# Kernel optimization log

Hardware: AMD Instinct MI355X
Metric: run time of the kernel (lower is better)

Reference implementation:

```python
import jax, jax.numpy as jnp
import numpy as np

# Config constants (match init_kwargs)
D_MODEL = 1024
D_MLP = 2048
NUM_EXPERTS = 8
EXPERTS_PER_TOKEN = 2
BATCH, SEQ = 2, 2048


def setup_inputs() -> dict:
    key = jax.random.key(0)
    k0, k1, k2, k3, k4 = jax.random.split(key, 5)
    init = lambda k, shape: jax.random.normal(k, shape, jnp.float32) * 0.02
    return {
        "x": jax.random.normal(k0, (BATCH, SEQ, D_MODEL), jnp.float32),
        "W_router": init(k1, (D_MODEL, NUM_EXPERTS)),
        "W_gate": init(k2, (NUM_EXPERTS, D_MODEL, D_MLP)),
        "W_in": init(k3, (NUM_EXPERTS, D_MODEL, D_MLP)),
        "W_out": init(k4, (NUM_EXPERTS, D_MLP, D_MODEL)),
    }


def reference(x, W_router, W_gate, W_in, W_out):
    B, S, D = x.shape
    h = x.reshape(-1, D)                                  # [T, D]
    T = h.shape[0]
    E = W_router.shape[1]

    # Router: softmax in fp32, top-k, renormalize (as in torch source)
    router_logits = h @ W_router                          # [T, E]
    probs = jax.nn.softmax(router_logits.astype(jnp.float32), axis=-1)
    top_w, top_i = jax.lax.top_k(probs, EXPERTS_PER_TOKEN)  # [T, K]
    top_w = top_w / top_w.sum(axis=-1, keepdims=True)
    top_w = top_w.astype(h.dtype)

    # Dense combine matrix [T, E]; top-k indices are distinct per token
    combine = jnp.zeros((T, E), h.dtype).at[jnp.arange(T)[:, None], top_i].set(top_w)

    # GatedMLP per expert: silu(h @ Wg) * (h @ Wi) @ Wo  (computed densely over experts,
    # then combined with the sparse routing weights -> same math as gather/MLP/scatter loop)
    gate_pre = jnp.einsum('td,edf->etf', h, W_gate)       # [E, T, F]
    up = jnp.einsum('td,edf->etf', h, W_in)               # [E, T, F]
    act = jax.nn.silu(gate_pre) * up                      # [E, T, F]
    expert_out = jnp.einsum('etf,efd->etd', act, W_out)   # [E, T, D]

    out = jnp.einsum('etd,te->td', expert_out, combine)   # [T, D]
    return out.reshape(B, S, D), router_logits
```

## Files before the change

### kernel.cpp

```cpp
#include <hip/hip_runtime.h>
#include <cstdint>
#include <cstddef>

#define T_TOK 4096
#define DM 1024
#define DF 2048
#define NE 8
#define PADROWS 9216
#define MAXTILES 72

typedef unsigned short u16;
typedef unsigned int u32;
using short8 = __attribute__((ext_vector_type(8))) short;
using f32x4  = __attribute__((ext_vector_type(4))) float;

static constexpr size_t OFF_H    = 0;
static constexpr size_t OFF_WGT  = OFF_H   + (size_t)T_TOK * DM * 2;
static constexpr size_t OFF_WIT  = OFF_WGT + (size_t)NE * DM * DF * 2;
static constexpr size_t OFF_WOT  = OFF_WIT + (size_t)NE * DM * DF * 2;
static constexpr size_t OFF_A    = OFF_WOT + (size_t)NE * DF * DM * 2;
static constexpr size_t OFF_TOK  = OFF_A   + (size_t)PADROWS * DF * 2;
static constexpr size_t OFF_WL   = OFF_TOK + PADROWS * 4;
static constexpr size_t OFF_TEXP = OFF_WL  + PADROWS * 4;
static constexpr size_t OFF_TW   = OFF_TEXP + (size_t)T_TOK * 2 * 4;
static constexpr size_t OFF_CNT  = OFF_TW  + (size_t)T_TOK * 2 * 4;
static constexpr size_t OFF_CUR  = OFF_CNT + 64;
static constexpr size_t OFF_NT   = OFF_CUR + 64;
static constexpr size_t OFF_TE   = OFF_NT  + 64;
static constexpr size_t OFF_TP   = OFF_TE  + 512;
static constexpr size_t OFF_ZPG  = OFF_TP  + 512;
static constexpr size_t OFF_POS  = OFF_ZPG + 4096;

__device__ __forceinline__ u16 f2bf(float f) {
  u32 u = __builtin_bit_cast(u32, f);
  u += 0x7FFFu + ((u >> 16) & 1u);
  return (u16)(u >> 16);
}

__device__ __forceinline__ void async16(const void* g, void* l) {
  __builtin_amdgcn_global_load_lds((__attribute__((address_space(1))) void*)(g),
                                   (__attribute__((address_space(3))) void*)(l),
                                   16, 0, 0);
}

__global__ void convert_x_k(const float4* __restrict__ x, u16* __restrict__ h) {
  size_t i = (size_t)blockIdx.x * 256 + threadIdx.x;
  float4 v = x[i];
  u32 lo = (u32)f2bf(v.x) | ((u32)f2bf(v.y) << 16);
  u32 hi = (u32)f2bf(v.z) | ((u32)f2bf(v.w) << 16);
  uint2 o; o.x = lo; o.y = hi;
  *(uint2*)&h[i * 4] = o;
}

__global__ void init_small_k(int* __restrict__ tok, float* __restrict__ wl,
                             int* __restrict__ cnt, u16* __restrict__ zpg) {
  int i = blockIdx.x * 256 + threadIdx.x;
  if (i < PADROWS) { tok[i] = -1; wl[i] = 0.f; }
  if (i < NE) cnt[i] = 0;
  if (i < 2048) zpg[i] = 0;
}

__global__ void transpose_w_k(const float* __restrict__ Wg, const float* __restrict__ Wi,
                              const float* __restrict__ Wo, u16* __restrict__ wgT,
                              u16* __restrict__ wiT, u16* __restrict__ woT) {
  __shared__ u16 lT[64][65];
  int bid = blockIdx.x;
  int mat = bid >> 12;
  int r = bid & 4095;
  const float* src; u16* dst; int R, C;
  if (mat == 0)      { src = Wg; dst = wgT; R = DM; C = DF; }
  else if (mat == 1) { src = Wi; dst = wiT; R = DM; C = DF; }
  else               { src = Wo; dst = woT; R = DF; C = DM; }
  int e = r >> 9;
  int rem = r & 511;
  int ctiles = C >> 6;
  int tr = rem / ctiles, tc = rem % ctiles;
  size_t eb = (size_t)e * R * C;
  int r0 = tr * 64, c0 = tc * 64;
  int wv = threadIdx.x >> 6, lane = threadIdx.x & 63;
#pragma unroll
  for (int it = 0; it < 16; ++it) {
    int rl = it * 4 + wv;
    float v = src[eb + (size_t)(r0 + rl) * C + c0 + lane];
    lT[lane][rl] = f2bf(v);
  }
  __syncthreads();
#pragma unroll
  for (int it = 0; it < 16; ++it) {
    int cl = it * 4 + wv;
    dst[eb + (size_t)(c0 + cl) * R + r0 + lane] = lT[cl][lane];
  }
}

__global__ void router_k(const float* __restrict__ x, const float* __restrict__ Wr,
                         float* __restrict__ logits, int* __restrict__ texp,
                         float* __restrict__ tw, int* __restrict__ cnt) {
  int wv = threadIdx.x >> 6, lane = threadIdx.x & 63;
  int t = blockIdx.x * 4 + wv;
  const float* h = x + (size_t)t * DM;
  float acc[8] = {0.f, 0.f, 0.f, 0.f, 0.f, 0.f, 0.f, 0.f};
#pragma unroll
  for (int j = 0; j < 16; ++j) {
    float hv = h[lane + j * 64];
    const float4* wr = (const float4*)(Wr + (size_t)(lane + j * 64) * 8);
    float4 w0 = wr[0], w1 = wr[1];
    acc[0] += hv * w0.x; acc[1] += hv * w0.y; acc[2] += hv * w0.z; acc[3] += hv * w0.w;
    acc[4] += hv * w1.x; acc[5] += hv * w1.y; acc[6] += hv * w1.z; acc[7] += hv * w1.w;
  }
#pragma unroll
  for (int e = 0; e < 8; ++e)
#pragma unroll
    for (int off = 32; off > 0; off >>= 1) acc[e] += __shfl_down(acc[e], off, 64);
  if (lane == 0) {
    float mx = acc[0];
#pragma unroll
    for (int e = 1; e < 8; ++e) mx = fmaxf(mx, acc[e]);
    float p[8];
#pragma unroll
    for (int e = 0; e < 8; ++e) p[e] = __expf(acc[e] - mx);
    int i1 = 0; float b1 = p[0];
#pragma unroll
    for (int e = 1; e < 8; ++e) if (p[e] > b1) { b1 = p[e]; i1 = e; }
    int i2 = -1; float b2 = -1.f;
#pragma unroll
    for (int e = 0; e < 8; ++e) if (e != i1 && p[e] > b2) { b2 = p[e]; i2 = e; }
    float inv = 1.f / (b1 + b2);
    texp[t * 2] = i1; texp[t * 2 + 1] = i2;
    tw[t * 2] = b1 * inv; tw[t * 2 + 1] = b2 * inv;
    atomicAdd(&cnt[i1], 1); atomicAdd(&cnt[i2], 1);
#pragma unroll
    for (int e = 0; e < 8; ++e) logits[(size_t)t * 8 + e] = acc[e];
  }
}

__global__ void plan_k(const int* __restrict__ cnt, int* __restrict__ cursor,
                       int* __restrict__ tile_e, int* __restrict__ tile_p,
                       int* __restrict__ ntiles) {
  if (threadIdx.x == 0) {
    int off = 0, nt = 0;
    for (int e = 0; e < NE; ++e) {
      cursor[e] = off;
      int n = cnt[e];
      int t = (n + 127) >> 7;
      for (int i = 0; i < t; ++i) { tile_e[nt] = e; tile_p[nt] = off + i * 128; ++nt; }
      off += t * 128;
    }
    *ntiles = nt;
  }
}

__global__ void scatter_k(const int* __restrict__ texp, const float* __restrict__ tw,
                          int* __restrict__ cursor, int* __restrict__ tok,
                          float* __restrict__ wl, int* __restrict__ pos) {
  int t = blockIdx.x * 256 + threadIdx.x;
#pragma unroll
  for (int k = 0; k < 2; ++k) {
    int e = texp[t * 2 + k];
    int p = atomicAdd(&cursor[e], 1);
    tok[p] = t;
    wl[p] = tw[t * 2 + k];
    pos[t * 2 + k] = p;
  }
}

__global__ __launch_bounds__(256) void gemm1_k(
    const u16* __restrict__ hbf, const u16* __restrict__ wgT, const u16* __restrict__ wiT,
    const int* __restrict__ tok, const float* __restrict__ wl,
    const int* __restrict__ tile_e, const int* __restrict__ tile_p,
    const int* __restrict__ ntiles, const u16* __restrict__ zpg,
    u16* __restrict__ Aact) {
  __shared__ char smem[65536];
  const int tile = blockIdx.y;
  if (tile >= *ntiles) return;
  const int e  = tile_e[tile];
  const int p0 = tile_p[tile];
  const int f0 = blockIdx.x * 64;
  const int tid = threadIdx.x, wv = tid >> 6, lane = tid & 63;

  const u16* hsrc[4];
  int hoff[4];
#pragma unroll
  for (int i = 0; i < 4; ++i) {
    const int row = wv * 32 + i * 8 + (lane >> 3);
    const int gc  = (lane & 7) ^ (row & 7);
    const int tk  = tok[p0 + row];
    hsrc[i] = (tk >= 0) ? (hbf + (size_t)tk * DM + gc * 8) : (zpg + gc * 8);
    hoff[i] = (wv * 32 + i * 8) * 64;
  }
  const u16* wbase = ((wv < 2) ? wgT : wiT) + (size_t)e * DM * DF;
  const int half = wv & 1, mt = wv >> 1;
  const u16* bsrc[4];
  int boff[4];
#pragma unroll
  for (int i = 0; i < 4; ++i) {
    const int row = half * 32 + i * 8 + (lane >> 3);
    const int gc  = (lane & 7) ^ (row & 7);
    bsrc[i] = wbase + (size_t)(f0 + row) * DM + gc * 8;
    boff[i] = 8192 + mt * 4096 + (half * 32 + i * 8) * 64;
  }

  f32x4 accG[4][2], accU[4][2];
#pragma unroll
  for (int m = 0; m < 4; ++m)
#pragma unroll
    for (int n = 0; n < 2; ++n) { accG[m][n] = (f32x4)(0.f); accU[m][n] = (f32x4)(0.f); }

  const int wr = wv >> 1, wc = wv & 1;
  const int wrBase = wr * 64, wcBase = wc * 32;
  const int l4 = lane >> 4, ln = lane & 15;

  {
    u16* b = (u16*)smem;
#pragma unroll
    for (int i = 0; i < 4; ++i) async16(hsrc[i], b + hoff[i]);
#pragma unroll
    for (int i = 0; i < 4; ++i) async16(bsrc[i], b + boff[i]);
  }
  __syncthreads();

  int cur = 0;
  for (int kt = 0; kt < DM / 64; ++kt) {
    if (kt < DM / 64 - 1) {
      u16* b = (u16*)smem + (cur ^ 1) * 16384;
#pragma unroll
      for (int i = 0; i < 4; ++i) async16(hsrc[i] + (size_t)(kt + 1) * 64, b + hoff[i]);
#pragma unroll
      for (int i = 0; i < 4; ++i) async16(bsrc[i] + (size_t)(kt + 1) * 64, b + boff[i]);
    }
    const u16* b = (const u16*)smem + cur * 16384;
#pragma unroll
    for (int s = 0; s < 2; ++s) {
      const int c = s * 4 + l4;
      short8 a[4], bg[2], bu[2];
#pragma unroll
      for (int m = 0; m < 4; ++m) {
        const int row = wrBase + m * 16 + ln;
        a[m] = *(const short8*)&b[row * 64 + ((c ^ (row & 7)) * 8)];
      }
#pragma unroll
      for (int n = 0; n < 2; ++n) {
        const int rowb = wcBase + n * 16 + ln;
        const int so = rowb * 64 + ((c ^ (rowb & 7)) * 8);
        bg[n] = *(const short8*)&b[8192 + so];
        bu[n] = *(const short8*)&b[12288 + so];
      }
#pragma unroll
      for (int m = 0; m < 4; ++m)
#pragma unroll
        for (int n = 0; n < 2; ++n) {
          accG[m][n] = __builtin_amdgcn_mfma_f32_16x16x32_bf16(a[m], bg[n], accG[m][n], 0, 0, 0);
          accU[m][n] = __builtin_amdgcn_mfma_f32_16x16x32_bf16(a[m], bu[n], accU[m][n], 0, 0, 0);
        }
    }
    __syncthreads();
    cur ^= 1;
  }

  u16* lOut = (u16*)smem;
#pragma unroll
  for (int m = 0; m < 4; ++m)
#pragma unroll
    for (int j = 0; j < 4; ++j) {
      const int row = wrBase + m * 16 + l4 * 4 + j;
      const float w = wl[p0 + row];
#pragma unroll
      for (int n = 0; n < 2; ++n) {
        const float g = accG[m][n][j];
        const float u = accU[m][n][j];
        const float val = (g / (1.f + __expf(-g))) * u * w;
        lOut[row * 80 + wcBase + n * 16 + ln] = f2bf(val);
      }
    }
  __syncthreads();
  const int r = tid >> 1, hf = tid & 1;
  u16* gdst = Aact + (size_t)(p0 + r) * DF + f0 + hf * 32;
  const u16* lsrc = &lOut[r * 80 + hf * 32];
#pragma unroll
  for (int i = 0; i < 4; ++i)
    *(short8*)(gdst + i * 8) = *(const short8*)(lsrc + i * 8);
}

__global__ __launch_bounds__(256) void gemm2_k(
    const u16* __restrict__ Aact, const u16* __restrict__ woT,
    const int* __restrict__ tile_e, const int* __restrict__ tile_p,
    const int* __restrict__ ntiles, float* __restrict__ scr) {
  __shared__ char smem[49152];
  const int tile = blockIdx.y;
  if (tile >= *ntiles) return;
  const int e  = tile_e[tile];
  const int p0 = tile_p[tile];
  const int d0 = blockIdx.x * 64;
  const int tid = threadIdx.x, wv = tid >> 6, lane = tid & 63;

  const u16* asrc[4];
  int aoff[4];
#pragma unroll
  for (int i = 0; i < 4; ++i) {
    const int row = wv * 32 + i * 8 + (lane >> 3);
    const int gc  = (lane & 7) ^ (row & 7);
    asrc[i] = Aact + (size_t)(p0 + row) * DF + gc * 8;
    aoff[i] = (wv * 32 + i * 8) * 64;
  }
  const u16* wb = woT + (size_t)e * DM * DF;
  const u16* wsrc[2];
  int woff[2];
#pragma unroll
  for (int i = 0; i < 2; ++i) {
    const int row = wv * 16 + i * 8 + (lane >> 3);
    const int gc  = (lane & 7) ^ (row & 7);
    wsrc[i] = wb + (size_t)(d0 + row) * DF + gc * 8;
    woff[i] = 8192 + (wv * 16 + i * 8) * 64;
  }

  f32x4 acc[4][2];
#pragma unroll
  for (int m = 0; m < 4; ++m)
#pragma unroll
    for (int n = 0; n < 2; ++n) acc[m][n] = (f32x4)(0.f);

  const int wr = wv >> 1, wc = wv & 1;
  const int wrBase = wr * 64, wcBase = wc * 32;
  const int l4 = lane >> 4, ln = lane & 15;

  {
    u16* b = (u16*)smem;
#pragma unroll
    for (int i = 0; i < 4; ++i) async16(asrc[i], b + aoff[i]);
#pragma unroll
    for (int i = 0; i < 2; ++i) async16(wsrc[i], b + woff[i]);
  }
  __syncthreads();

  int cur = 0;
  for (int kt = 0; kt < DF / 64; ++kt) {
    if (kt < DF / 64 - 1) {
      u16* b = (u16*)smem + (cur ^ 1) * 12288;
#pragma unroll
      for (int i = 0; i < 4; ++i) async16(asrc[i] + (size_t)(kt + 1) * 64, b + aoff[i]);
#pragma unroll
      for (int i = 0; i < 2; ++i) async16(wsrc[i] + (size_t)(kt + 1) * 64, b + woff[i]);
    }
    const u16* b = (const u16*)smem + cur * 12288;
#pragma unroll
    for (int s = 0; s < 2; ++s) {
      const int c = s * 4 + l4;
      short8 a[4], bw[2];
#pragma unroll
      for (int m = 0; m < 4; ++m) {
        const int row = wrBase + m * 16 + ln;
        a[m] = *(const short8*)&b[row * 64 + ((c ^ (row & 7)) * 8)];
      }
#pragma unroll
      for (int n = 0; n < 2; ++n) {
        const int rowb = wcBase + n * 16 + ln;
        bw[n] = *(const short8*)&b[8192 + rowb * 64 + ((c ^ (rowb & 7)) * 8)];
      }
#pragma unroll
      for (int m = 0; m < 4; ++m)
#pragma unroll
        for (int n = 0; n < 2; ++n)
          acc[m][n] = __builtin_amdgcn_mfma_f32_16x16x32_bf16(a[m], bw[n], acc[m][n], 0, 0, 0);
    }
    __syncthreads();
    cur ^= 1;
  }

#pragma unroll
  for (int m = 0; m < 4; ++m)
#pragma unroll
    for (int j = 0; j < 4; ++j) {
      const int row = wrBase + m * 16 + l4 * 4 + j;
      float* dst = scr + (size_t)(p0 + row) * DM + d0;
#pragma unroll
      for (int n = 0; n < 2; ++n)
        dst[wcBase + n * 16 + ln] = acc[m][n][j];
    }
}

__global__ void combine_k(const float* __restrict__ scr, const int* __restrict__ pos,
                          float* __restrict__ out) {
  const int t = blockIdx.x;
  const int d = threadIdx.x;
  const int p1 = pos[t * 2], p2 = pos[t * 2 + 1];
  const float4 a = *(const float4*)(scr + (size_t)p1 * DM + d * 4);
  const float4 b = *(const float4*)(scr + (size_t)p2 * DM + d * 4);
  float4 o;
  o.x = a.x + b.x; o.y = a.y + b.y; o.z = a.z + b.z; o.w = a.w + b.w;
  *(float4*)(out + (size_t)t * DM + d * 4) = o;
}

extern "C" void kernel_launch(void* const* d_in, const int* in_sizes, int n_in,
                              void* d_out, int out_size, void* d_ws, size_t ws_size,
                              hipStream_t stream) {
  const float* x  = (const float*)d_in[0];
  const float* Wr = (const float*)d_in[1];
  const float* Wg = (const float*)d_in[2];
  const float* Wi = (const float*)d_in[3];
  const float* Wo = (const float*)d_in[4];
  float* outF = (float*)d_out;
  float* logits = outF + (size_t)T_TOK * DM;

  char* ws = (char*)d_ws;
  u16*  hbf   = (u16*)(ws + OFF_H);
  u16*  wgT   = (u16*)(ws + OFF_WGT);
  u16*  wiT   = (u16*)(ws + OFF_WIT);
  u16*  woT   = (u16*)(ws + OFF_WOT);
  u16*  Aact  = (u16*)(ws + OFF_A);
  int*  tok   = (int*)(ws + OFF_TOK);
  float* wl   = (float*)(ws + OFF_WL);
  int*  texp  = (int*)(ws + OFF_TEXP);
  float* tw   = (float*)(ws + OFF_TW);
  int*  cnt   = (int*)(ws + OFF_CNT);
  int*  cur   = (int*)(ws + OFF_CUR);
  int*  nt    = (int*)(ws + OFF_NT);
  int*  te    = (int*)(ws + OFF_TE);
  int*  tp    = (int*)(ws + OFF_TP);
  u16*  zpg   = (u16*)(ws + OFF_ZPG);
  int*  pos   = (int*)(ws + OFF_POS);
  float* scr  = (float*)(ws + OFF_WGT);

  convert_x_k<<<4096, 256, 0, stream>>>((const float4*)x, hbf);
  init_small_k<<<40, 256, 0, stream>>>(tok, wl, cnt, zpg);
  transpose_w_k<<<12288, 256, 0, stream>>>(Wg, Wi, Wo, wgT, wiT, woT);
  router_k<<<1024, 256, 0, stream>>>(x, Wr, logits, texp, tw, cnt);
  plan_k<<<1, 64, 0, stream>>>(cnt, cur, te, tp, nt);
  scatter_k<<<16, 256, 0, stream>>>(texp, tw, cur, tok, wl, pos);
  gemm1_k<<<dim3(DF / 64, MAXTILES), 256, 0, stream>>>(hbf, wgT, wiT, tok, wl, te, tp, nt, zpg, Aact);
  gemm2_k<<<dim3(DM / 64, MAXTILES), 256, 0, stream>>>(Aact, woT, te, tp, nt, scr);
  combine_k<<<4096, 256, 0, stream>>>(scr, pos, outF);
}
```

Before: 351.3 us.

## Fuse x conversion into router, vectorize transpose stores, bf16 scratch output

```diff
diff --git a/kernel.cpp b/kernel.cpp
--- a/kernel.cpp
+++ b/kernel.cpp
@@ -28,14 +28,17 @@
 static constexpr size_t OFF_NT   = OFF_CUR + 64;
 static constexpr size_t OFF_TE   = OFF_NT  + 64;
 static constexpr size_t OFF_TP   = OFF_TE  + 512;
-static constexpr size_t OFF_ZPG  = OFF_TP  + 512;
-static constexpr size_t OFF_POS  = OFF_ZPG + 4096;
+static constexpr size_t OFF_POS  = OFF_TP  + 512;
 
 __device__ __forceinline__ u16 f2bf(float f) {
   u32 u = __builtin_bit_cast(u32, f);
   u += 0x7FFFu + ((u >> 16) & 1u);
   return (u16)(u >> 16);
 }
+__device__ __forceinline__ float bf2f(u16 b) {
+  u32 u = ((u32)b) << 16;
+  return __builtin_bit_cast(float, u);
+}
 
 __device__ __forceinline__ void async16(const void* g, void* l) {
   __builtin_amdgcn_global_load_lds((__attribute__((address_space(1))) void*)(g),
@@ -43,21 +46,11 @@
                                    16, 0, 0);
 }
 
-__global__ void convert_x_k(const float4* __restrict__ x, u16* __restrict__ h) {
-  size_t i = (size_t)blockIdx.x * 256 + threadIdx.x;
-  float4 v = x[i];
-  u32 lo = (u32)f2bf(v.x) | ((u32)f2bf(v.y) << 16);
-  u32 hi = (u32)f2bf(v.z) | ((u32)f2bf(v.w) << 16);
-  uint2 o; o.x = lo; o.y = hi;
-  *(uint2*)&h[i * 4] = o;
-}
-
 __global__ void init_small_k(int* __restrict__ tok, float* __restrict__ wl,
-                             int* __restrict__ cnt, u16* __restrict__ zpg) {
+                             int* __restrict__ cnt) {
   int i = blockIdx.x * 256 + threadIdx.x;
   if (i < PADROWS) { tok[i] = -1; wl[i] = 0.f; }
   if (i < NE) cnt[i] = 0;
-  if (i < 2048) zpg[i] = 0;
 }
 
 __global__ void transpose_w_k(const float* __restrict__ Wg, const float* __restrict__ Wi,
@@ -86,22 +79,29 @@
   }
   __syncthreads();
 #pragma unroll
-  for (int it = 0; it < 16; ++it) {
-    int cl = it * 4 + wv;
-    dst[eb + (size_t)(c0 + cl) * R + r0 + lane] = lT[cl][lane];
+  for (int i = 0; i < 2; ++i) {
+    const int cl = i * 32 + wv * 8 + (lane >> 3);
+    const int b8 = (lane & 7) * 8;
+    u16 tmp[8];
+#pragma unroll
+    for (int k = 0; k < 8; ++k) tmp[k] = lT[cl][b8 + k];
+    *(short8*)&dst[eb + (size_t)(c0 + cl) * R + r0 + b8] = *(const short8*)tmp;
   }
 }
 
 __global__ void router_k(const float* __restrict__ x, const float* __restrict__ Wr,
                          float* __restrict__ logits, int* __restrict__ texp,
-                         float* __restrict__ tw, int* __restrict__ cnt) {
+                         float* __restrict__ tw, int* __restrict__ cnt,
+                         u16* __restrict__ hbf) {
   int wv = threadIdx.x >> 6, lane = threadIdx.x & 63;
   int t = blockIdx.x * 4 + wv;
   const float* h = x + (size_t)t * DM;
+  u16* hb = hbf + (size_t)t * DM;
   float acc[8] = {0.f, 0.f, 0.f, 0.f, 0.f, 0.f, 0.f, 0.f};
 #pragma unroll
   for (int j = 0; j < 16; ++j) {
     float hv = h[lane + j * 64];
+    hb[lane + j * 64] = f2bf(hv);
     const float4* wr = (const float4*)(Wr + (size_t)(lane + j * 64) * 8);
     float4 w0 = wr[0], w1 = wr[1];
     acc[0] += hv * w0.x; acc[1] += hv * w0.y; acc[2] += hv * w0.z; acc[3] += hv * w0.w;
@@ -136,16 +136,23 @@
 __global__ void plan_k(const int* __restrict__ cnt, int* __restrict__ cursor,
                        int* __restrict__ tile_e, int* __restrict__ tile_p,
                        int* __restrict__ ntiles) {
-  if (threadIdx.x == 0) {
-    int off = 0, nt = 0;
+  __shared__ int toff[NE + 1], roff[NE];
+  const int l = threadIdx.x;
+  if (l == 0) {
+    int o = 0, nt = 0;
     for (int e = 0; e < NE; ++e) {
-      cursor[e] = off;
-      int n = cnt[e];
-      int t = (n + 127) >> 7;
-      for (int i = 0; i < t; ++i) { tile_e[nt] = e; tile_p[nt] = off + i * 128; ++nt; }
-      off += t * 128;
-    }
+      int t = (cnt[e] + 127) >> 7;
+      cursor[e] = o; toff[e] = nt; roff[e] = o;
+      nt += t; o += t * 128;
+    }
+    toff[NE] = nt;
     *ntiles = nt;
+  }
+  __syncthreads();
+  for (int idx = l; idx < MAXTILES; idx += 64) {
+    int e = 0;
+    while (e < NE && !(idx >= toff[e] && idx < toff[e + 1])) ++e;
+    if (e < NE) { tile_e[idx] = e; tile_p[idx] = roff[e] + (idx - toff[e]) * 128; }
   }
 }
 
@@ -167,8 +174,7 @@
     const u16* __restrict__ hbf, const u16* __restrict__ wgT, const u16* __restrict__ wiT,
     const int* __restrict__ tok, const float* __restrict__ wl,
     const int* __restrict__ tile_e, const int* __restrict__ tile_p,
-    const int* __restrict__ ntiles, const u16* __restrict__ zpg,
-    u16* __restrict__ Aact) {
+    const int* __restrict__ ntiles, u16* __restrict__ Aact) {
   __shared__ char smem[65536];
   const int tile = blockIdx.y;
   if (tile >= *ntiles) return;
@@ -183,8 +189,9 @@
   for (int i = 0; i < 4; ++i) {
     const int row = wv * 32 + i * 8 + (lane >> 3);
     const int gc  = (lane & 7) ^ (row & 7);
-    const int tk  = tok[p0 + row];
-    hsrc[i] = (tk >= 0) ? (hbf + (size_t)tk * DM + gc * 8) : (zpg + gc * 8);
+    int tk  = tok[p0 + row];
+    if (tk < 0) tk = 0;
+    hsrc[i] = hbf + (size_t)tk * DM + gc * 8;
     hoff[i] = (wv * 32 + i * 8) * 64;
   }
   const u16* wbase = ((wv < 2) ? wgT : wiT) + (size_t)e * DM * DF;
@@ -283,7 +290,7 @@
 __global__ __launch_bounds__(256) void gemm2_k(
     const u16* __restrict__ Aact, const u16* __restrict__ woT,
     const int* __restrict__ tile_e, const int* __restrict__ tile_p,
-    const int* __restrict__ ntiles, float* __restrict__ scr) {
+    const int* __restrict__ ntiles, u16* __restrict__ scr) {
   __shared__ char smem[49152];
   const int tile = blockIdx.y;
   if (tile >= *ntiles) return;
@@ -365,27 +372,37 @@
     cur ^= 1;
   }
 
+  u16* lOut = (u16*)smem;
 #pragma unroll
   for (int m = 0; m < 4; ++m)
 #pragma unroll
     for (int j = 0; j < 4; ++j) {
       const int row = wrBase + m * 16 + l4 * 4 + j;
-      float* dst = scr + (size_t)(p0 + row) * DM + d0;
 #pragma unroll
       for (int n = 0; n < 2; ++n)
-        dst[wcBase + n * 16 + ln] = acc[m][n][j];
-    }
-}
-
-__global__ void combine_k(const float* __restrict__ scr, const int* __restrict__ pos,
+        lOut[row * 72 + wcBase + n * 16 + ln] = f2bf(acc[m][n][j]);
+    }
+  __syncthreads();
+  const int r = tid >> 1, hf = tid & 1;
+  u16* gdst = scr + (size_t)(p0 + r) * DM + d0 + hf * 32;
+  const u16* lsrc = &lOut[r * 72 + hf * 32];
+#pragma unroll
+  for (int i = 0; i < 4; ++i)
+    *(short8*)(gdst + i * 8) = *(const short8*)(lsrc + i * 8);
+}
+
+__global__ void combine_k(const u16* __restrict__ scr, const int* __restrict__ pos,
                           float* __restrict__ out) {
   const int t = blockIdx.x;
   const int d = threadIdx.x;
   const int p1 = pos[t * 2], p2 = pos[t * 2 + 1];
-  const float4 a = *(const float4*)(scr + (size_t)p1 * DM + d * 4);
-  const float4 b = *(const float4*)(scr + (size_t)p2 * DM + d * 4);
+  const ushort4 a = *(const ushort4*)(scr + (size_t)p1 * DM + d * 4);
+  const ushort4 b = *(const ushort4*)(scr + (size_t)p2 * DM + d * 4);
   float4 o;
-  o.x = a.x + b.x; o.y = a.y + b.y; o.z = a.z + b.z; o.w = a.w + b.w;
+  o.x = bf2f(a.x) + bf2f(b.x);
+  o.y = bf2f(a.y) + bf2f(b.y);
+  o.z = bf2f(a.z) + bf2f(b.z);
+  o.w = bf2f(a.w) + bf2f(b.w);
   *(float4*)(out + (size_t)t * DM + d * 4) = o;
 }
 
@@ -415,17 +432,15 @@
   int*  nt    = (int*)(ws + OFF_NT);
   int*  te    = (int*)(ws + OFF_TE);
   int*  tp    = (int*)(ws + OFF_TP);
-  u16*  zpg   = (u16*)(ws + OFF_ZPG);
   int*  pos   = (int*)(ws + OFF_POS);
-  float* scr  = (float*)(ws + OFF_WGT);
-
-  convert_x_k<<<4096, 256, 0, stream>>>((const float4*)x, hbf);
-  init_small_k<<<40, 256, 0, stream>>>(tok, wl, cnt, zpg);
+  u16*  scr   = (u16*)(ws + OFF_WGT);
+
+  init_small_k<<<40, 256, 0, stream>>>(tok, wl, cnt);
   transpose_w_k<<<12288, 256, 0, stream>>>(Wg, Wi, Wo, wgT, wiT, woT);
-  router_k<<<1024, 256, 0, stream>>>(x, Wr, logits, texp, tw, cnt);
+  router_k<<<1024, 256, 0, stream>>>(x, Wr, logits, texp, tw, cnt, hbf);
   plan_k<<<1, 64, 0, stream>>>(cnt, cur, te, tp, nt);
   scatter_k<<<16, 256, 0, stream>>>(texp, tw, cur, tok, wl, pos);
-  gemm1_k<<<dim3(DF / 64, MAXTILES), 256, 0, stream>>>(hbf, wgT, wiT, tok, wl, te, tp, nt, zpg, Aact);
+  gemm1_k<<<dim3(DF / 64, MAXTILES), 256, 0, stream>>>(hbf, wgT, wiT, tok, wl, te, tp, nt, Aact);
   gemm2_k<<<dim3(DM / 64, MAXTILES), 256, 0, stream>>>(Aact, woT, te, tp, nt, scr);
   combine_k<<<4096, 256, 0, stream>>>(scr, pos, outF);
 }
```

Result: no change. 347.1 us (-1.2%).
